# Optimization experiments

Measured on AMD Instinct MI355X. Metric: run time of the kernel, lower is better.

The kernel has to match this reference:

```python
import jax, jax.numpy as jnp
import numpy as np
import math

NUM_HEADS = 8

def setup_inputs() -> dict:
    key = jax.random.key(0)
    ks = jax.random.split(key, 5)
    b, h, w, c = 4, 128, 128, 256
    x = jax.random.normal(ks[0], (b, h, w, c), dtype=jnp.float32)
    scale = 1.0 / math.sqrt(c)  # keep weights reasonably scaled (kaiming-like)
    Wq = jax.random.normal(ks[1], (c, c), dtype=jnp.float32) * scale
    Wk = jax.random.normal(ks[2], (c, c), dtype=jnp.float32) * scale
    Wv = jax.random.normal(ks[3], (c, c), dtype=jnp.float32) * scale
    Wout = jax.random.normal(ks[4], (c, c), dtype=jnp.float32) * scale
    return {"x": x, "Wq": Wq, "Wk": Wk, "Wv": Wv, "Wout": Wout}

def reference(x, Wq, Wk, Wv, Wout):
    b, h, w, c = x.shape
    hw = h * w
    heads = NUM_HEADS
    dh = c // heads
    xs = x.reshape(b, hw, c)
    q = xs @ Wq  # (b, hw, c)
    k = xs @ Wk
    v = xs @ Wv

    def split_heads(t):
        # (b, hw, c) -> (b, c, hw) -> (b, heads, dh, hw)
        return t.transpose(0, 2, 1).reshape(b, heads, dh, hw)

    q = split_heads(q)
    k = split_heads(k)
    v = split_heads(v)
    # L2-normalize along the feature (hw) axis; original has no epsilon
    q = q / jnp.linalg.norm(q, axis=-1, keepdims=True)
    k = k / jnp.linalg.norm(k, axis=-1, keepdims=True)
    d_k = q.shape[-1]  # = hw
    attn = jnp.einsum('bhcd,bhed->bhce', q, k) / math.sqrt(d_k)  # (b,heads,dh,dh)
    attn = jax.nn.softmax(attn, axis=-1)
    vals = jnp.einsum('bhce,bhed->bhcd', attn, v)  # (b,heads,dh,hw)
    vals = vals.transpose(0, 3, 1, 2).reshape(b, hw, c)
    out = (vals @ Wout).reshape(b, h, w, c)
    return out
```

## Files before the change

kernel.cpp:

```cpp
#include <hip/hip_runtime.h>


#define B_   4
#define HW_  16384
#define C_   256

typedef __attribute__((ext_vector_type(8))) short short8;
typedef __attribute__((ext_vector_type(4))) float floatx4;

__device__ __forceinline__ unsigned short f2bf(float f) {
  unsigned u = __builtin_bit_cast(unsigned, f);
  u += 0x7FFFu + ((u >> 16) & 1u);
  return (unsigned short)(u >> 16);
}

__device__ __forceinline__ void gl_lds16(const unsigned short* g, unsigned short* l) {
  __builtin_amdgcn_global_load_lds(
      (const __attribute__((address_space(1))) unsigned int*)g,
      (__attribute__((address_space(3))) unsigned int*)l, 16, 0, 0);
}

__global__ __launch_bounds__(256) void k_cast_tr(const float* __restrict__ x,
                                                 unsigned short* __restrict__ xb,
                                                 unsigned short* __restrict__ xT) {
  __shared__ unsigned short lds[64][72];
  int bid = blockIdx.x;
  int t = threadIdx.x;
  int ct = bid & 3;
  int pt = (bid >> 2) & 255;
  int b  = bid >> 10;
  const float* src = x + ((size_t)(b * HW_ + pt * 64)) * C_ + ct * 64;
#pragma unroll
  for (int e = 0; e < 4; e++) {
    int lin = t + e * 256;
    int p = lin >> 4, c4 = lin & 15;
    float4 v = *(const float4*)(src + (size_t)p * C_ + c4 * 4);
    ushort4 h;
    h.x = f2bf(v.x); h.y = f2bf(v.y); h.z = f2bf(v.z); h.w = f2bf(v.w);
    *(ushort4*)(xb + ((size_t)(b * HW_ + pt * 64 + p)) * C_ + ct * 64 + c4 * 4) = h;
    lds[c4 * 4 + 0][p] = h.x;
    lds[c4 * 4 + 1][p] = h.y;
    lds[c4 * 4 + 2][p] = h.z;
    lds[c4 * 4 + 3][p] = h.w;
  }
  __syncthreads();
#pragma unroll
  for (int e = 0; e < 4; e++) {
    int lin = t + e * 256;
    int c = lin >> 4, p4 = lin & 15;
    ushort4 h;
    h.x = lds[c][p4 * 4 + 0];
    h.y = lds[c][p4 * 4 + 1];
    h.z = lds[c][p4 * 4 + 2];
    h.w = lds[c][p4 * 4 + 3];
    *(ushort4*)(xT + ((size_t)(b * C_ + ct * 64 + c)) * HW_ + pt * 64 + p4 * 4) = h;
  }
}

__global__ __launch_bounds__(256) void k_sgemm(const unsigned short* __restrict__ xT,
                                               float* __restrict__ part) {
  __shared__ unsigned short At[128 * 256];
  __shared__ unsigned short Bt[128 * 256];
  int bid = blockIdx.x;
  int ks = bid & 31, nt = (bid >> 5) & 1, mt = (bid >> 6) & 1, b = bid >> 7;
  const unsigned short* Ab = xT + ((size_t)(b * C_ + mt * 128)) * HW_ + ks * 512;
  const unsigned short* Bb = xT + ((size_t)(b * C_ + nt * 128)) * HW_ + ks * 512;
  int t = threadIdx.x, lane = t & 63, w = t >> 6;
  int wm = w >> 1, wn = w & 1;
  int l15 = lane & 15, l4 = lane >> 4;
  int lrow = lane >> 5;
  int lslot = lane & 31;
  floatx4 acc[4][4];
  floatx4 z = {0.f, 0.f, 0.f, 0.f};
#pragma unroll
  for (int i = 0; i < 4; i++)
#pragma unroll
    for (int j = 0; j < 4; j++) acc[i][j] = z;

  for (int ph = 0; ph < 2; ph++) {
    if (ph) __syncthreads();
#pragma unroll
    for (int i = 0; i < 16; i++) {
      int issue = w * 16 + i;
      int row = issue * 2 + lrow;
      int goct = lslot ^ (row & 31);
      gl_lds16(Ab + (size_t)row * HW_ + ph * 256 + goct * 8, At + issue * 512);
      gl_lds16(Bb + (size_t)row * HW_ + ph * 256 + goct * 8, Bt + issue * 512);
    }
    __syncthreads();
#pragma unroll
    for (int kk = 0; kk < 8; kk++) {
      short8 af[4], bfv[4];
      int oct = kk * 4 + l4;
#pragma unroll
      for (int tm = 0; tm < 4; tm++) {
        int row = wm * 64 + tm * 16 + l15;
        af[tm] = *(const short8*)(At + row * 256 + ((oct ^ (row & 31)) * 8));
      }
#pragma unroll
      for (int tn = 0; tn < 4; tn++) {
        int row = wn * 64 + tn * 16 + l15;
        bfv[tn] = *(const short8*)(Bt + row * 256 + ((oct ^ (row & 31)) * 8));
      }
#pragma unroll
      for (int tm = 0; tm < 4; tm++)
#pragma unroll
        for (int tn = 0; tn < 4; tn++)
          acc[tm][tn] = __builtin_amdgcn_mfma_f32_16x16x32_bf16(af[tm], bfv[tn],
                                                                acc[tm][tn], 0, 0, 0);
    }
  }
  float* pb = part + (size_t)bid * 16384;
#pragma unroll
  for (int tm = 0; tm < 4; tm++)
#pragma unroll
    for (int tn = 0; tn < 4; tn++)
#pragma unroll
      for (int r = 0; r < 4; r++) {
        int m = wm * 64 + tm * 16 + l4 * 4 + r;
        int n = wn * 64 + tn * 16 + l15;
        pb[m * 128 + n] = acc[tm][tn][r];
      }
}

__global__ __launch_bounds__(256) void k_sred(const float* __restrict__ part,
                                              float* __restrict__ S) {
  int idx = blockIdx.x * 256 + threadIdx.x;
  int b = idx >> 16;
  int m = (idx >> 8) & 255, n = idx & 255;
  const float* p = part + ((size_t)((b * 4 + (m >> 7) * 2 + (n >> 7)) * 32)) * 16384
                   + (m & 127) * 128 + (n & 127);
  float s = 0.f;
#pragma unroll
  for (int k = 0; k < 32; k++) s += p[k * 16384];
  S[idx] = s;
}

__global__ __launch_bounds__(256) void k_gemm_sw(const float* __restrict__ S,
                                                 const float* __restrict__ Wq,
                                                 const float* __restrict__ Wk,
                                                 float* __restrict__ SWq,
                                                 float* __restrict__ SWk) {
  __shared__ float As[64][17];
  __shared__ float Bs[16][65];
  int bid = blockIdx.x;
  int nt = bid & 7, mt = (bid >> 3) & 3, b = bid >> 5;
  int mb = mt * 64;
  const float* Wsel = (nt < 4) ? Wq : Wk;
  int nb = (nt & 3) * 64;
  int t = threadIdx.x, tx = t & 15, ty = t >> 4;
  float acc[4][4] = {};
  for (int kt = 0; kt < 16; kt++) {
    {
      int row = t >> 2, kq = t & 3;
      float4 v = *(const float4*)(S + ((size_t)(b * C_ + mb + row)) * C_ + kt * 16 + kq * 4);
      As[row][kq * 4 + 0] = v.x; As[row][kq * 4 + 1] = v.y;
      As[row][kq * 4 + 2] = v.z; As[row][kq * 4 + 3] = v.w;
    }
    {
      int kk = t >> 4, n4 = t & 15;
      float4 v = *(const float4*)(Wsel + ((size_t)(kt * 16 + kk)) * C_ + nb + n4 * 4);
      Bs[kk][n4 * 4 + 0] = v.x; Bs[kk][n4 * 4 + 1] = v.y;
      Bs[kk][n4 * 4 + 2] = v.z; Bs[kk][n4 * 4 + 3] = v.w;
    }
    __syncthreads();
#pragma unroll
    for (int k = 0; k < 16; k++) {
      float a[4], bb[4];
#pragma unroll
      for (int i = 0; i < 4; i++) a[i] = As[ty * 4 + i][k];
#pragma unroll
      for (int j = 0; j < 4; j++) bb[j] = Bs[k][tx * 4 + j];
#pragma unroll
      for (int i = 0; i < 4; i++)
#pragma unroll
        for (int j = 0; j < 4; j++) acc[i][j] += a[i] * bb[j];
    }
    __syncthreads();
  }
#pragma unroll
  for (int i = 0; i < 4; i++)
#pragma unroll
    for (int j = 0; j < 4; j++) {
      int row = mb + ty * 4 + i;
      int ng = nt * 64 + tx * 4 + j;
      if (ng < 256) SWq[((size_t)(b * C_ + row)) * C_ + ng] = acc[i][j];
      else          SWk[((size_t)(b * C_ + row)) * C_ + ng - 256] = acc[i][j];
    }
}

__global__ __launch_bounds__(256) void k_fuse(const float* __restrict__ Wq,
                                              const float* __restrict__ Wk,
                                              const float* __restrict__ SWq,
                                              const float* __restrict__ SWk,
                                              const float* __restrict__ Wout,
                                              float* __restrict__ U) {
  __shared__ float Wqh[256][32];
  __shared__ float Wkh[256][32];
  __shared__ float SWqh[256][32];
  __shared__ float SWkh[256][32];
  __shared__ float Lg[32][33];
  __shared__ float qp[8][32], kp[8][32], qin[32], kin[32];
  int b = blockIdx.x >> 3, h = blockIdx.x & 7;
  int t = threadIdx.x;
  int col = t & 31, rgrp = t >> 5;
  for (int r0 = 0; r0 < 256; r0 += 8) {
    int row = r0 + rgrp;
    Wqh[row][col]  = Wq[(size_t)row * C_ + h * 32 + col];
    Wkh[row][col]  = Wk[(size_t)row * C_ + h * 32 + col];
    SWqh[row][col] = SWq[((size_t)(b * C_ + row)) * C_ + h * 32 + col];
    SWkh[row][col] = SWk[((size_t)(b * C_ + row)) * C_ + h * 32 + col];
  }
  __syncthreads();
  {
    float g[4] = {0.f, 0.f, 0.f, 0.f};
    for (int k = 0; k < 256; k++) {
      float swk = SWkh[k][col];
#pragma unroll
      for (int r = 0; r < 4; r++) g[r] += Wqh[k][rgrp + 8 * r] * swk;
    }
#pragma unroll
    for (int r = 0; r < 4; r++) Lg[rgrp + 8 * r][col] = g[r];
  }
  {
    float sq = 0.f, sk = 0.f;
    for (int k = rgrp * 32; k < rgrp * 32 + 32; k++) {
      sq += Wqh[k][col] * SWqh[k][col];
      sk += Wkh[k][col] * SWkh[k][col];
    }
    qp[rgrp][col] = sq;
    kp[rgrp][col] = sk;
  }
  __syncthreads();
  if (t < 32) {
    float a = 0.f;
#pragma unroll
    for (int p = 0; p < 8; p++) a += qp[p][t];
    qin[t] = rsqrtf(a);
  } else if (t < 64) {
    int j = t - 32;
    float a = 0.f;
#pragma unroll
    for (int p = 0; p < 8; p++) a += kp[p][j];
    kin[j] = rsqrtf(a);
  }
  __syncthreads();
  if (t < 32) {
    float row[32];
    float mx = -1e30f;
#pragma unroll
    for (int j = 0; j < 32; j++) {
      row[j] = Lg[t][j] * qin[t] * kin[j] * 0.0078125f;
      mx = fmaxf(mx, row[j]);
    }
    float sum = 0.f;
#pragma unroll
    for (int j = 0; j < 32; j++) { row[j] = __expf(row[j] - mx); sum += row[j]; }
    float inv = 1.0f / sum;
#pragma unroll
    for (int j = 0; j < 32; j++) Lg[t][j] = row[j] * inv;
  }
  __syncthreads();
  float (*Wo)[256] = reinterpret_cast<float(*)[256]>(&Wqh[0][0]);
#pragma unroll
  for (int r = 0; r < 32; r++) Wo[r][t] = Wout[((size_t)(h * 32 + r)) * C_ + t];
  __syncthreads();
  for (int j = 0; j < 32; j++) {
    float a = 0.f;
#pragma unroll
    for (int i2 = 0; i2 < 32; i2++) a += Lg[i2][j] * Wo[i2][t];
    U[((size_t)(b * C_ + h * 32 + j)) * C_ + t] = a;
  }
}

__global__ __launch_bounds__(256) void k_gemm_w3(const float* __restrict__ Wv,
                                                 const float* __restrict__ U,
                                                 unsigned short* __restrict__ W3bT) {
  __shared__ float As[64][17];
  __shared__ float Bs[16][65];
  int bid = blockIdx.x;
  int nt = bid & 3, mt = (bid >> 2) & 3, b = bid >> 4;
  int mb = mt * 64, nb = nt * 64;
  int t = threadIdx.x, tx = t & 15, ty = t >> 4;
  float acc[4][4] = {};
  for (int kt = 0; kt < 16; kt++) {
    {
      int row = t >> 2, kq = t & 3;
      float4 v = *(const float4*)(Wv + ((size_t)(mb + row)) * C_ + kt * 16 + kq * 4);
      As[row][kq * 4 + 0] = v.x; As[row][kq * 4 + 1] = v.y;
      As[row][kq * 4 + 2] = v.z; As[row][kq * 4 + 3] = v.w;
    }
    {
      int kk = t >> 4, n4 = t & 15;
      float4 v = *(const float4*)(U + ((size_t)(b * C_ + kt * 16 + kk)) * C_ + nb + n4 * 4);
      Bs[kk][n4 * 4 + 0] = v.x; Bs[kk][n4 * 4 + 1] = v.y;
      Bs[kk][n4 * 4 + 2] = v.z; Bs[kk][n4 * 4 + 3] = v.w;
    }
    __syncthreads();
#pragma unroll
    for (int k = 0; k < 16; k++) {
      float a[4], bb[4];
#pragma unroll
      for (int i = 0; i < 4; i++) a[i] = As[ty * 4 + i][k];
#pragma unroll
      for (int j = 0; j < 4; j++) bb[j] = Bs[k][tx * 4 + j];
#pragma unroll
      for (int i = 0; i < 4; i++)
#pragma unroll
        for (int j = 0; j < 4; j++) acc[i][j] += a[i] * bb[j];
    }
    __syncthreads();
  }
#pragma unroll
  for (int i = 0; i < 4; i++)
#pragma unroll
    for (int j = 0; j < 4; j++)
      W3bT[((size_t)(b * C_ + nb + tx * 4 + j)) * C_ + mb + ty * 4 + i] = f2bf(acc[i][j]);
}

__global__ __launch_bounds__(256) void k_out(const unsigned short* __restrict__ xb,
                                             const unsigned short* __restrict__ W3bT,
                                             float* __restrict__ out) {
  __shared__ unsigned short At[128 * 64];
  __shared__ unsigned short Bt[128 * 64];
  int bid = blockIdx.x;
  int ntile = bid & 1, mtile = bid >> 1;
  int b = mtile >> 7;
  const unsigned short* Ab = xb + (size_t)mtile * 128 * C_;
  const unsigned short* Bb = W3bT + ((size_t)(b * C_ + ntile * 128)) * C_;
  int t = threadIdx.x, lane = t & 63, w = t >> 6;
  int wm = w >> 1, wn = w & 1;
  int l8 = lane >> 3, l7 = lane & 7;
  int srcoct = l7 ^ l8;
  int l15 = lane & 15, l4 = lane >> 4;
  floatx4 acc[4][4];
  floatx4 z = {0.f, 0.f, 0.f, 0.f};
#pragma unroll
  for (int i = 0; i < 4; i++)
#pragma unroll
    for (int j = 0; j < 4; j++) acc[i][j] = z;
  for (int s = 0; s < 4; s++) {
    if (s) __syncthreads();
#pragma unroll
    for (int i = 0; i < 4; i++) {
      int gi = w * 4 + i;
      int row = gi * 8 + l8;
      gl_lds16(Ab + (size_t)row * C_ + s * 64 + srcoct * 8, At + gi * 512);
      gl_lds16(Bb + (size_t)row * C_ + s * 64 + srcoct * 8, Bt + gi * 512);
    }
    __syncthreads();
#pragma unroll
    for (int kk = 0; kk < 2; kk++) {
      short8 af[4], bfv[4];
#pragma unroll
      for (int tm = 0; tm < 4; tm++) {
        int row = wm * 64 + tm * 16 + l15;
        int oct = kk * 4 + l4;
        af[tm] = *(const short8*)(At + row * 64 + ((oct ^ (l15 & 7)) * 8));
      }
#pragma unroll
      for (int tn = 0; tn < 4; tn++) {
        int row = wn * 64 + tn * 16 + l15;
        int oct = kk * 4 + l4;
        bfv[tn] = *(const short8*)(Bt + row * 64 + ((oct ^ (l15 & 7)) * 8));
      }
#pragma unroll
      for (int tm = 0; tm < 4; tm++)
#pragma unroll
        for (int tn = 0; tn < 4; tn++)
          acc[tm][tn] = __builtin_amdgcn_mfma_f32_16x16x32_bf16(af[tm], bfv[tn],
                                                                acc[tm][tn], 0, 0, 0);
    }
  }
  float* ob = out + (size_t)mtile * 128 * C_ + ntile * 128;
#pragma unroll
  for (int tm = 0; tm < 4; tm++)
#pragma unroll
    for (int tn = 0; tn < 4; tn++)
#pragma unroll
      for (int r = 0; r < 4; r++) {
        int m = wm * 64 + tm * 16 + l4 * 4 + r;
        int n = wn * 64 + tn * 16 + l15;
        ob[(size_t)m * C_ + n] = acc[tm][tn][r];
      }
}

extern "C" void kernel_launch(void* const* d_in, const int* in_sizes, int n_in,
                              void* d_out, int out_size, void* d_ws, size_t ws_size,
                              hipStream_t stream) {
  const float* x    = (const float*)d_in[0];
  const float* Wq   = (const float*)d_in[1];
  const float* Wk   = (const float*)d_in[2];
  const float* Wv   = (const float*)d_in[3];
  const float* Wout = (const float*)d_in[4];
  float* out = (float*)d_out;

  unsigned short* xT = (unsigned short*)d_ws;
  unsigned short* xb = xT + (size_t)16777216;
  float* part = (float*)(xb + (size_t)16777216);
  float* S    = part + (size_t)8388608;
  float* SWq  = S + 262144;
  float* SWk  = SWq + 262144;
  float* U    = SWk + 262144;
  unsigned short* W3bT = (unsigned short*)(U + 262144);

  k_cast_tr<<<dim3(4096), dim3(256), 0, stream>>>(x, xb, xT);
  k_sgemm<<<dim3(512), dim3(256), 0, stream>>>(xT, part);
  k_sred<<<dim3(1024), dim3(256), 0, stream>>>(part, S);
  k_gemm_sw<<<dim3(128), dim3(256), 0, stream>>>(S, Wq, Wk, SWq, SWk);
  k_fuse<<<dim3(32), dim3(256), 0, stream>>>(Wq, Wk, SWq, SWk, Wout, U);
  k_gemm_w3<<<dim3(64), dim3(256), 0, stream>>>(Wv, U, W3bT);
  k_out<<<dim3(1024), dim3(256), 0, stream>>>(xb, W3bT, out);
}
```

Before: 231.8 us.

## Compute full symmetric Gram tile per block and widen output GEMM tiles

The Gram-matrix kernel now loads one 256-row panel of xT into shared memory and computes the full 256x256 block from it with 512 threads. Previously separate A and B panels were loaded per 128x128 quadrant, so the same data was fetched twice. The output GEMM now covers all 256 columns per block, halving redundant loads of the x tile. The small FP32 GEMMs get transposed LDS tiles so reads can be float4 vectorized. The risk is fewer blocks (128 and 512), leaving many CUs idle in the Gram kernel, plus higher register pressure from 32 accumulators.

```diff
diff --git a/kernel.cpp b/kernel.cpp
--- a/kernel.cpp
+++ b/kernel.cpp
@@ -57,69 +57,65 @@
   }
 }
 
-__global__ __launch_bounds__(256) void k_sgemm(const unsigned short* __restrict__ xT,
+__global__ __launch_bounds__(512) void k_sgemm(const unsigned short* __restrict__ xT,
                                                float* __restrict__ part) {
-  __shared__ unsigned short At[128 * 256];
-  __shared__ unsigned short Bt[128 * 256];
+  __shared__ unsigned short Pt[256 * 128];
   int bid = blockIdx.x;
-  int ks = bid & 31, nt = (bid >> 5) & 1, mt = (bid >> 6) & 1, b = bid >> 7;
-  const unsigned short* Ab = xT + ((size_t)(b * C_ + mt * 128)) * HW_ + ks * 512;
-  const unsigned short* Bb = xT + ((size_t)(b * C_ + nt * 128)) * HW_ + ks * 512;
+  int ks = bid & 31, b = bid >> 5;
+  const unsigned short* Pb = xT + ((size_t)b * C_) * HW_ + ks * 512;
   int t = threadIdx.x, lane = t & 63, w = t >> 6;
-  int wm = w >> 1, wn = w & 1;
+  int wq = w >> 1, h = w & 1;
+  int wm = wq >> 1, wn = wq & 1;
   int l15 = lane & 15, l4 = lane >> 4;
-  int lrow = lane >> 5;
-  int lslot = lane & 31;
-  floatx4 acc[4][4];
+  floatx4 acc[4][8];
   floatx4 z = {0.f, 0.f, 0.f, 0.f};
 #pragma unroll
   for (int i = 0; i < 4; i++)
 #pragma unroll
-    for (int j = 0; j < 4; j++) acc[i][j] = z;
-
-  for (int ph = 0; ph < 2; ph++) {
+    for (int j = 0; j < 8; j++) acc[i][j] = z;
+
+  for (int ph = 0; ph < 4; ph++) {
     if (ph) __syncthreads();
 #pragma unroll
-    for (int i = 0; i < 16; i++) {
-      int issue = w * 16 + i;
-      int row = issue * 2 + lrow;
-      int goct = lslot ^ (row & 31);
-      gl_lds16(Ab + (size_t)row * HW_ + ph * 256 + goct * 8, At + issue * 512);
-      gl_lds16(Bb + (size_t)row * HW_ + ph * 256 + goct * 8, Bt + issue * 512);
-    }
-    __syncthreads();
-#pragma unroll
-    for (int kk = 0; kk < 8; kk++) {
-      short8 af[4], bfv[4];
+    for (int i = 0; i < 8; i++) {
+      int issue = w * 8 + i;
+      int row = issue * 4 + l4;
+      int goct = l15 ^ (row & 15);
+      gl_lds16(Pb + (size_t)row * HW_ + ph * 128 + goct * 8, Pt + issue * 512);
+    }
+    __syncthreads();
+#pragma unroll
+    for (int kk = 0; kk < 4; kk++) {
+      short8 af[4], bfv[8];
       int oct = kk * 4 + l4;
 #pragma unroll
       for (int tm = 0; tm < 4; tm++) {
-        int row = wm * 64 + tm * 16 + l15;
-        af[tm] = *(const short8*)(At + row * 256 + ((oct ^ (row & 31)) * 8));
-      }
-#pragma unroll
-      for (int tn = 0; tn < 4; tn++) {
-        int row = wn * 64 + tn * 16 + l15;
-        bfv[tn] = *(const short8*)(Bt + row * 256 + ((oct ^ (row & 31)) * 8));
+        int row = wm * 128 + h * 64 + tm * 16 + l15;
+        af[tm] = *(const short8*)(Pt + row * 128 + ((oct ^ (row & 15)) * 8));
+      }
+#pragma unroll
+      for (int tn = 0; tn < 8; tn++) {
+        int row = wn * 128 + tn * 16 + l15;
+        bfv[tn] = *(const short8*)(Pt + row * 128 + ((oct ^ (row & 15)) * 8));
       }
 #pragma unroll
       for (int tm = 0; tm < 4; tm++)
 #pragma unroll
-        for (int tn = 0; tn < 4; tn++)
+        for (int tn = 0; tn < 8; tn++)
           acc[tm][tn] = __builtin_amdgcn_mfma_f32_16x16x32_bf16(af[tm], bfv[tn],
                                                                 acc[tm][tn], 0, 0, 0);
     }
   }
-  float* pb = part + (size_t)bid * 16384;
+  float* pb = part + (size_t)(b * 32 + ks) * 65536;
 #pragma unroll
   for (int tm = 0; tm < 4; tm++)
 #pragma unroll
-    for (int tn = 0; tn < 4; tn++)
+    for (int tn = 0; tn < 8; tn++)
 #pragma unroll
       for (int r = 0; r < 4; r++) {
-        int m = wm * 64 + tm * 16 + l4 * 4 + r;
-        int n = wn * 64 + tn * 16 + l15;
-        pb[m * 128 + n] = acc[tm][tn][r];
+        int m = wm * 128 + h * 64 + tm * 16 + l4 * 4 + r;
+        int n = wn * 128 + tn * 16 + l15;
+        pb[m * 256 + n] = acc[tm][tn][r];
       }
 }
 
@@ -127,12 +123,11 @@
                                               float* __restrict__ S) {
   int idx = blockIdx.x * 256 + threadIdx.x;
   int b = idx >> 16;
-  int m = (idx >> 8) & 255, n = idx & 255;
-  const float* p = part + ((size_t)((b * 4 + (m >> 7) * 2 + (n >> 7)) * 32)) * 16384
-                   + (m & 127) * 128 + (n & 127);
+  int mn = idx & 65535;
+  const float* p = part + ((size_t)b << 21) + mn;
   float s = 0.f;
 #pragma unroll
-  for (int k = 0; k < 32; k++) s += p[k * 16384];
+  for (int k = 0; k < 32; k++) s += p[(size_t)k << 16];
   S[idx] = s;
 }
 
@@ -141,8 +136,8 @@
                                                  const float* __restrict__ Wk,
                                                  float* __restrict__ SWq,
                                                  float* __restrict__ SWk) {
-  __shared__ float As[64][17];
-  __shared__ float Bs[16][65];
+  __shared__ float Ast[16][68];
+  __shared__ float Bs[16][68];
   int bid = blockIdx.x;
   int nt = bid & 7, mt = (bid >> 3) & 3, b = bid >> 5;
   int mb = mt * 64;
@@ -154,23 +149,21 @@
     {
       int row = t >> 2, kq = t & 3;
       float4 v = *(const float4*)(S + ((size_t)(b * C_ + mb + row)) * C_ + kt * 16 + kq * 4);
-      As[row][kq * 4 + 0] = v.x; As[row][kq * 4 + 1] = v.y;
-      As[row][kq * 4 + 2] = v.z; As[row][kq * 4 + 3] = v.w;
+      Ast[kq * 4 + 0][row] = v.x; Ast[kq * 4 + 1][row] = v.y;
+      Ast[kq * 4 + 2][row] = v.z; Ast[kq * 4 + 3][row] = v.w;
     }
     {
       int kk = t >> 4, n4 = t & 15;
       float4 v = *(const float4*)(Wsel + ((size_t)(kt * 16 + kk)) * C_ + nb + n4 * 4);
-      Bs[kk][n4 * 4 + 0] = v.x; Bs[kk][n4 * 4 + 1] = v.y;
-      Bs[kk][n4 * 4 + 2] = v.z; Bs[kk][n4 * 4 + 3] = v.w;
+      *(float4*)&Bs[kk][n4 * 4] = v;
     }
     __syncthreads();
 #pragma unroll
     for (int k = 0; k < 16; k++) {
-      float a[4], bb[4];
-#pragma unroll
-      for (int i = 0; i < 4; i++) a[i] = As[ty * 4 + i][k];
-#pragma unroll
-      for (int j = 0; j < 4; j++) bb[j] = Bs[k][tx * 4 + j];
+      float4 a4 = *(const float4*)&Ast[k][ty * 4];
+      float4 b4 = *(const float4*)&Bs[k][tx * 4];
+      float a[4] = {a4.x, a4.y, a4.z, a4.w};
+      float bb[4] = {b4.x, b4.y, b4.z, b4.w};
 #pragma unroll
       for (int i = 0; i < 4; i++)
 #pragma unroll
@@ -276,8 +269,8 @@
 __global__ __launch_bounds__(256) void k_gemm_w3(const float* __restrict__ Wv,
                                                  const float* __restrict__ U,
                                                  unsigned short* __restrict__ W3bT) {
-  __shared__ float As[64][17];
-  __shared__ float Bs[16][65];
+  __shared__ float Ast[16][68];
+  __shared__ float Bs[16][68];
   int bid = blockIdx.x;
   int nt = bid & 3, mt = (bid >> 2) & 3, b = bid >> 4;
   int mb = mt * 64, nb = nt * 64;
@@ -287,23 +280,21 @@
     {
       int row = t >> 2, kq = t & 3;
       float4 v = *(const float4*)(Wv + ((size_t)(mb + row)) * C_ + kt * 16 + kq * 4);
-      As[row][kq * 4 + 0] = v.x; As[row][kq * 4 + 1] = v.y;
-      As[row][kq * 4 + 2] = v.z; As[row][kq * 4 + 3] = v.w;
+      Ast[kq * 4 + 0][row] = v.x; Ast[kq * 4 + 1][row] = v.y;
+      Ast[kq * 4 + 2][row] = v.z; Ast[kq * 4 + 3][row] = v.w;
     }
     {
       int kk = t >> 4, n4 = t & 15;
       float4 v = *(const float4*)(U + ((size_t)(b * C_ + kt * 16 + kk)) * C_ + nb + n4 * 4);
-      Bs[kk][n4 * 4 + 0] = v.x; Bs[kk][n4 * 4 + 1] = v.y;
-      Bs[kk][n4 * 4 + 2] = v.z; Bs[kk][n4 * 4 + 3] = v.w;
+      *(float4*)&Bs[kk][n4 * 4] = v;
     }
     __syncthreads();
 #pragma unroll
     for (int k = 0; k < 16; k++) {
-      float a[4], bb[4];
-#pragma unroll
-      for (int i = 0; i < 4; i++) a[i] = As[ty * 4 + i][k];
-#pragma unroll
-      for (int j = 0; j < 4; j++) bb[j] = Bs[k][tx * 4 + j];
+      float4 a4 = *(const float4*)&Ast[k][ty * 4];
+      float4 b4 = *(const float4*)&Bs[k][tx * 4];
+      float a[4] = {a4.x, a4.y, a4.z, a4.w};
+      float bb[4] = {b4.x, b4.y, b4.z, b4.w};
 #pragma unroll
       for (int i = 0; i < 4; i++)
 #pragma unroll
@@ -322,65 +313,68 @@
                                              const unsigned short* __restrict__ W3bT,
                                              float* __restrict__ out) {
   __shared__ unsigned short At[128 * 64];
-  __shared__ unsigned short Bt[128 * 64];
-  int bid = blockIdx.x;
-  int ntile = bid & 1, mtile = bid >> 1;
+  __shared__ unsigned short Bt[256 * 64];
+  int mtile = blockIdx.x;
   int b = mtile >> 7;
   const unsigned short* Ab = xb + (size_t)mtile * 128 * C_;
-  const unsigned short* Bb = W3bT + ((size_t)(b * C_ + ntile * 128)) * C_;
+  const unsigned short* Bb = W3bT + (size_t)b * C_ * C_;
   int t = threadIdx.x, lane = t & 63, w = t >> 6;
-  int wm = w >> 1, wn = w & 1;
+  int h = w >> 1, c2 = w & 1;
   int l8 = lane >> 3, l7 = lane & 7;
   int srcoct = l7 ^ l8;
   int l15 = lane & 15, l4 = lane >> 4;
-  floatx4 acc[4][4];
+  floatx4 acc[4][8];
   floatx4 z = {0.f, 0.f, 0.f, 0.f};
 #pragma unroll
   for (int i = 0; i < 4; i++)
 #pragma unroll
-    for (int j = 0; j < 4; j++) acc[i][j] = z;
+    for (int j = 0; j < 8; j++) acc[i][j] = z;
   for (int s = 0; s < 4; s++) {
     if (s) __syncthreads();
 #pragma unroll
     for (int i = 0; i < 4; i++) {
-      int gi = w * 4 + i;
-      int row = gi * 8 + l8;
-      gl_lds16(Ab + (size_t)row * C_ + s * 64 + srcoct * 8, At + gi * 512);
-      gl_lds16(Bb + (size_t)row * C_ + s * 64 + srcoct * 8, Bt + gi * 512);
+      int ia = w * 4 + i;
+      int row = ia * 8 + l8;
+      gl_lds16(Ab + (size_t)row * C_ + s * 64 + srcoct * 8, At + ia * 512);
+    }
+#pragma unroll
+    for (int i = 0; i < 8; i++) {
+      int ib = w * 8 + i;
+      int row = ib * 8 + l8;
+      gl_lds16(Bb + (size_t)row * C_ + s * 64 + srcoct * 8, Bt + ib * 512);
     }
     __syncthreads();
 #pragma unroll
     for (int kk = 0; kk < 2; kk++) {
-      short8 af[4], bfv[4];
+      short8 af[4], bfv[8];
+      int oct = kk * 4 + l4;
 #pragma unroll
       for (int tm = 0; tm < 4; tm++) {
-        int row = wm * 64 + tm * 16 + l15;
-        int oct = kk * 4 + l4;
-        af[tm] = *(const short8*)(At + row * 64 + ((oct ^ (l15 & 7)) * 8));
-      }
-#pragma unroll
-      for (int tn = 0; tn < 4; tn++) {
-        int row = wn * 64 + tn * 16 + l15;
-        int oct = kk * 4 + l4;
-        bfv[tn] = *(const short8*)(Bt + row * 64 + ((oct ^ (l15 & 7)) * 8));
+        int row = h * 64 + tm * 16 + l15;
+        af[tm] = *(const short8*)(At + row * 64 + ((oct ^ (row & 7)) * 8));
+      }
+#pragma unroll
+      for (int tn = 0; tn < 8; tn++) {
+        int row = c2 * 128 + tn * 16 + l15;
+        bfv[tn] = *(const short8*)(Bt + row * 64 + ((oct ^ (row & 7)) * 8));
       }
 #pragma unroll
       for (int tm = 0; tm < 4; tm++)
 #pragma unroll
-        for (int tn = 0; tn < 4; tn++)
+        for (int tn = 0; tn < 8; tn++)
           acc[tm][tn] = __builtin_amdgcn_mfma_f32_16x16x32_bf16(af[tm], bfv[tn],
                                                                 acc[tm][tn], 0, 0, 0);
     }
   }
-  float* ob = out + (size_t)mtile * 128 * C_ + ntile * 128;
+  float* ob = out + (size_t)mtile * 128 * C_;
 #pragma unroll
   for (int tm = 0; tm < 4; tm++)
 #pragma unroll
-    for (int tn = 0; tn < 4; tn++)
+    for (int tn = 0; tn < 8; tn++)
 #pragma unroll
       for (int r = 0; r < 4; r++) {
-        int m = wm * 64 + tm * 16 + l4 * 4 + r;
-        int n = wn * 64 + tn * 16 + l15;
+        int m = h * 64 + tm * 16 + l4 * 4 + r;
+        int n = c2 * 128 + tn * 16 + l15;
         ob[(size_t)m * C_ + n] = acc[tm][tn][r];
       }
 }
@@ -405,10 +399,10 @@
   unsigned short* W3bT = (unsigned short*)(U + 262144);
 
   k_cast_tr<<<dim3(4096), dim3(256), 0, stream>>>(x, xb, xT);
-  k_sgemm<<<dim3(512), dim3(256), 0, stream>>>(xT, part);
+  k_sgemm<<<dim3(128), dim3(512), 0, stream>>>(xT, part);
   k_sred<<<dim3(1024), dim3(256), 0, stream>>>(part, S);
   k_gemm_sw<<<dim3(128), dim3(256), 0, stream>>>(S, Wq, Wk, SWq, SWk);
   k_fuse<<<dim3(32), dim3(256), 0, stream>>>(Wq, Wk, SWq, SWk, Wout, U);
   k_gemm_w3<<<dim3(64), dim3(256), 0, stream>>>(Wv, U, W3bT);
-  k_out<<<dim3(1024), dim3(256), 0, stream>>>(xb, W3bT, out);
-}
+  k_out<<<dim3(512), dim3(256), 0, stream>>>(xb, W3bT, out);
+}
```

Result: no change. 232.0 us (+0.1%).
